# Kernel optimization log

Hardware: AMD Instinct MI355X
Metric: run time of the kernel (lower is better)

The kernel has to match this reference:

```python
import jax, jax.numpy as jnp
import numpy as np

NB, B, L, D, H = 4, 4, 1024, 512, 8
E = D // H  # head dim = 64
SCALE = 1.0 / np.sqrt(E)


def setup_inputs() -> dict:
    key = jax.random.key(0)
    ks = jax.random.split(key, 18)
    w = lambda k, shape: (jax.random.normal(k, shape, dtype=jnp.float32) * 0.02)
    inp = {
        'x': jax.random.normal(ks[0], (NB, B, L, D), dtype=jnp.float32),
        # per-block intra-attention projections, stored [in, out] (x @ W + b)
        'Wq': w(ks[1], (NB, D, D)), 'bq': w(ks[2], (NB, D)),
        'Wk': w(ks[3], (NB, D, D)), 'bk': w(ks[4], (NB, D)),
        'Wv': w(ks[5], (NB, D, D)), 'bv': w(ks[6], (NB, D)),
        'Wo': w(ks[7], (NB, D, D)), 'bo': w(ks[8], (NB, D)),
        # shared inter (router) attention projections
        'iWq': w(ks[9], (D, D)), 'ibq': w(ks[10], (D,)),
        'iWk': w(ks[11], (D, D)), 'ibk': w(ks[12], (D,)),
        'iWv': w(ks[13], (D, D)), 'ibv': w(ks[14], (D,)),
        'iWo': w(ks[15], (D, D)), 'ibo': w(ks[16], (D,)),
    }
    return inp


def _full_attn(q, k, v):
    # q,k,v: [..., S, H, E] with batch dims leading; unmasked FullAttention
    scores = jnp.einsum('...lhe,...she->...hls', q, k) * SCALE
    A = jax.nn.softmax(scores, axis=-1)
    return jnp.einsum('...hls,...shd->...lhd', A, v)


def reference(x, Wq, bq, Wk, bk, Wv, bv, Wo, bo,
              iWq, ibq, iWk, ibk, iWv, ibv, iWo, ibo):
    # ---- intra attention, vectorized over the NB blocks ----
    proj = lambda W, b: (jnp.einsum('nbld,nde->nble', x, W) + b[:, None, None, :])
    q = proj(Wq, bq).reshape(NB, B, L, H, E)
    k = proj(Wk, bk).reshape(NB, B, L, H, E)
    v = proj(Wv, bv).reshape(NB, B, L, H, E)
    o = _full_attn(q, k, v).reshape(NB, B, L, D)
    x_intra = jnp.einsum('nbld,nde->nble', o, Wo) + bo[:, None, None, :]

    # ---- inter attention over router tokens (last token of each block) ----
    routers = jnp.transpose(x_intra[:, :, -1, :], (1, 0, 2))  # [B, NB, D]
    rq = (routers @ iWq + ibq).reshape(B, NB, H, E)
    rk = (routers @ iWk + ibk).reshape(B, NB, H, E)
    rv = (routers @ iWv + ibv).reshape(B, NB, H, E)
    ro = _full_attn(rq, rk, rv).reshape(B, NB, D)
    x_inter = ro @ iWo + ibo  # [B, NB, D]

    # replace each block's last (router) token with its inter-attended version
    x_out = x_intra.at[:, :, -1, :].set(jnp.transpose(x_inter, (1, 0, 2)))
    return x_out  # [NB, B, L, D]
```

## Files before the change

### kernel.cpp

```cpp
#include <hip/hip_runtime.h>
#include <math.h>

#define NBV 4
#define BBV 4
#define LLV 1024
#define DDV 512
#define HHV 8
#define EEV 64

typedef unsigned short u16;
typedef _Float16 half8 __attribute__((ext_vector_type(8)));
typedef float f32x4 __attribute__((ext_vector_type(4)));

#define QSCALE 0.1803368801111243f

__device__ __forceinline__ u16 f2h(float f) {
  union { _Float16 h; u16 u; } v; v.h = (_Float16)f; return v.u;
}
__device__ __forceinline__ unsigned pkrtz(float a, float b) {
  typedef __fp16 fp16x2 __attribute__((ext_vector_type(2)));
  union { fp16x2 h; unsigned u; } c;
  c.h = __builtin_amdgcn_cvt_pkrtz(a, b);
  return c.u;
}
__device__ __forceinline__ void gload16(const void* g, void* l) {
  __builtin_amdgcn_global_load_lds(
      (const __attribute__((address_space(1))) unsigned int*)g,
      (__attribute__((address_space(3))) unsigned int*)l, 16, 0, 0);
}

__global__ __launch_bounds__(256) void convert(
    const float* __restrict__ x,
    const float* __restrict__ Wq, const float* __restrict__ Wk,
    const float* __restrict__ Wv, const float* __restrict__ Wo,
    u16* __restrict__ x_t, u16* __restrict__ wt, u16* __restrict__ wo)
{
  const int bid = blockIdx.x;
  if (bid < 4096) {
    const int t = bid * 256 + threadIdx.x;
    const int lane = t & 63;
    const int f = (t >> 6) & 7;
    const int kt = (t >> 9) & 15;
    const int rt = t >> 13;
    const int r = rt * 128 + f * 16 + (lane & 15);
    const int k0 = kt * 32 + (lane >> 4) * 8;
    const float* s = x + (size_t)r * 512 + k0;
    float4 v0 = *(const float4*)s;
    float4 v1 = *(const float4*)(s + 4);
    float vv[8] = {v0.x, v0.y, v0.z, v0.w, v1.x, v1.y, v1.z, v1.w};
    union { u16 s16[8]; uint4 v; } H;
#pragma unroll
    for (int j = 0; j < 8; ++j) H.s16[j] = f2h(vv[j]);
    *(uint4*)(x_t + (size_t)t * 8) = H.v;
  } else {
    const int qkv = (bid < 5632);
    const int t = (qkv ? (bid - 4096) : (bid - 5632)) * 256 + threadIdx.x;
    const int z = t >> 15;
    const int tl = t & 32767;
    const int lane = tl & 63;
    const int f = (tl >> 6) & 7;
    const int kt = (tl >> 9) & 15;
    const int rt = tl >> 13;
    const float* W;
    u16* dst;
    if (qkv) {
      const int nb = z / 3, p = z - nb * 3;
      W = (p == 0 ? Wq : p == 1 ? Wk : Wv) + (size_t)nb * 262144;
      dst = wt;
    } else {
      W = Wo + (size_t)z * 262144;
      dst = wo;
    }
    const int r = rt * 128 + f * 16 + (lane & 15);
    const int k0 = kt * 32 + (lane >> 4) * 8;
    union { u16 s16[8]; uint4 v; } H;
#pragma unroll
    for (int j = 0; j < 8; ++j) H.s16[j] = f2h(W[(size_t)(k0 + j) * 512 + r]);
    *(uint4*)(dst + (size_t)z * 262144 + (size_t)tl * 8) = H.v;
  }
}

template <int MODE>
__global__ __launch_bounds__(256) void gemm_f16(
    const u16* __restrict__ Aw, const u16* __restrict__ Bx,
    const float* __restrict__ bias0, const float* __restrict__ bias1,
    const float* __restrict__ bias2,
    u16* __restrict__ q_b, u16* __restrict__ k_b, u16* __restrict__ v_t,
    float* __restrict__ Cout)
{
  __shared__ __align__(16) u16 SM[17408];
  u16* As = SM;
  u16* Bs = SM + 4096;

  const int tid = threadIdx.x;
  const int lane = tid & 63, w = tid >> 6;
  const int l15 = lane & 15, l4 = lane >> 4;
  const int bid = blockIdx.x;

  int mt, nt, z;
  if (MODE == 0) {
    const int wgid = (bid & 7) * 192 + (bid >> 3);
    mt = wgid & 3; nt = (wgid >> 2) & 31; z = wgid >> 7;
  } else {
    const int wgid = (bid & 7) * 64 + (bid >> 3);
    mt = wgid & 31; nt = (wgid >> 5) & 3; z = wgid >> 7;
  }

  int nb, p;
  const u16 *A, *B;
  if (MODE == 0) {
    nb = z / 3; p = z - nb * 3;
    A = Aw + (size_t)z * 262144;
    B = Bx + (size_t)nb * 2097152;
  } else {
    nb = z; p = 0;
    A = Aw + (size_t)z * 2097152;
    B = Bx + (size_t)z * 262144;
  }

  const f32x4 z4 = {0.f, 0.f, 0.f, 0.f};
  f32x4 acc[4][4];
#pragma unroll
  for (int i = 0; i < 4; ++i)
#pragma unroll
    for (int j = 0; j < 4; ++j) acc[i][j] = z4;

  for (int kt = 0; kt < 16; ++kt) {
    const u16* ap = A + ((size_t)(mt * 16 + kt) * 8 + w * 2) * 512 + lane * 8;
    const u16* bp = B + ((size_t)(nt * 16 + kt) * 8 + w * 2) * 512 + lane * 8;
    __syncthreads();
    gload16(ap,       As + (w * 2 + 0) * 512);
    gload16(ap + 512, As + (w * 2 + 1) * 512);
    gload16(bp,       Bs + (w * 2 + 0) * 512);
    gload16(bp + 512, Bs + (w * 2 + 1) * 512);
    __syncthreads();

    half8 a[4], b[4];
#pragma unroll
    for (int m = 0; m < 4; ++m)
      a[m] = *(const half8*)(As + ((w >> 1) * 4 + m) * 512 + lane * 8);
#pragma unroll
    for (int n = 0; n < 4; ++n)
      b[n] = *(const half8*)(Bs + ((w & 1) * 4 + n) * 512 + lane * 8);
#pragma unroll
    for (int m = 0; m < 4; ++m)
#pragma unroll
      for (int n = 0; n < 4; ++n)
        acc[m][n] = __builtin_amdgcn_mfma_f32_16x16x32_f16(a[m], b[n], acc[m][n], 0, 0, 0);
  }

  if (MODE == 0) {
    const float* bias = (p == 0 ? bias0 : p == 1 ? bias1 : bias2) + nb * 512;
    const int hh = w >> 1;
    __syncthreads();
    if (p < 2) {
      const float scl = (p == 0) ? QSCALE : 1.0f;
#pragma unroll
      for (int mm = 0; mm < 4; ++mm) {
        const int c = mm * 4 + l4;
#pragma unroll
        for (int nn = 0; nn < 4; ++nn) {
          const int tok = (w & 1) * 64 + nn * 16 + l15;
          ushort4 pk;
#pragma unroll
          for (int i = 0; i < 4; ++i) {
            const int mf = mt * 128 + hh * 64 + mm * 16 + l4 * 4 + i;
            ((u16*)&pk)[i] = f2h((acc[mm][nn][i] + bias[mf]) * scl);
          }
          *(ushort4*)((char*)SM + hh * 17408 + tok * 136 +
                      ((c ^ (tok & 15)) * 8)) = pk;
        }
      }
      __syncthreads();
      u16* dst = (p == 0 ? q_b : k_b);
#pragma unroll
      for (int i = 0; i < 16; ++i) {
        const int idx = i * 256 + tid;
        const int h2 = idx >> 11, tok = (idx >> 4) & 127, c = idx & 15;
        ushort4 v = *(const ushort4*)((char*)SM + h2 * 17408 + tok * 136 +
                                      ((c ^ (tok & 15)) * 8));
        const int ltok = nt * 128 + tok;
        const int headf = (nb * 4 + (ltok >> 10)) * 8 + mt * 2 + h2;
        *(ushort4*)(dst + (size_t)headf * 65536 + (ltok & 1023) * 64 + c * 4) = v;
      }
    } else {
#pragma unroll
      for (int mm = 0; mm < 4; ++mm) {
#pragma unroll
        for (int nn = 0; nn < 4; ++nn) {
          const int tok = (w & 1) * 64 + nn * 16 + l15;
#pragma unroll
          for (int r = 0; r < 4; ++r) {
            const int e = mm * 16 + l4 * 4 + r;
            const int mf = mt * 128 + hh * 64 + e;
            *(u16*)((char*)SM + hh * 17408 + e * 264 + tok * 2) =
                f2h(acc[mm][nn][r] + bias[mf]);
          }
        }
      }
      __syncthreads();
#pragma unroll
      for (int i = 0; i < 16; ++i) {
        const int idx = i * 256 + tid;
        const int h2 = idx >> 11, rem = idx & 2047;
        const int e = rem >> 5, s = rem & 31;
        uint2 v = *(const uint2*)((char*)SM + h2 * 17408 + e * 264 + s * 8);
        const int headf = (nb * 4 + (nt >> 3)) * 8 + mt * 2 + h2;
        *(uint2*)(v_t + (size_t)headf * 65536 + e * 1024 +
                  (nt & 7) * 128 + s * 4) = v;
      }
    }
  } else {
#pragma unroll
    for (int mm = 0; mm < 4; ++mm) {
#pragma unroll
      for (int nn = 0; nn < 4; ++nn) {
        const int m0 = mt * 128 + ((w >> 1) * 4 + mm) * 16 + l4 * 4;
        const int n  = nt * 128 + ((w & 1) * 4 + nn) * 16 + l15;
        const float bz = bias0[nb * 512 + n];
#pragma unroll
        for (int r = 0; r < 4; ++r)
          Cout[((size_t)nb * 4096 + m0 + r) * 512 + n] = acc[mm][nn][r] + bz;
      }
    }
  }
}

__global__ __launch_bounds__(512, 4) void attn_mfma(
    const u16* __restrict__ Qb, const u16* __restrict__ Kb,
    const u16* __restrict__ Vt, u16* __restrict__ o_t)
{
  __shared__ __align__(16) u16 SM[26624];
  u16* KL = SM;
  u16* VL = SM + 8192;
  u16* PL = SM + 16384;

  const int tid = threadIdx.x;
  const int lane = tid & 63, w = tid >> 6;
  const int l15 = lane & 15, l4 = lane >> 4;
  const int sb = blockIdx.x;
  const int head = sb & 127;
  const int qt = sb >> 7;
  const size_t hbase = (size_t)head * 65536;
  const int q0 = qt * 256;

  half8 qf[2][2];
#pragma unroll
  for (int qm = 0; qm < 2; ++qm) {
    const u16* qp = Qb + hbase + (size_t)(q0 + w * 32 + qm * 16 + l15) * 64 + l4 * 8;
    qf[qm][0] = *(const half8*)qp;
    qf[qm][1] = *(const half8*)(qp + 32);
  }

  const f32x4 z4 = {0.f, 0.f, 0.f, 0.f};
  const _Float16 one_h = (_Float16)1.0f;
  const half8 ones = {one_h, one_h, one_h, one_h, one_h, one_h, one_h, one_h};
  f32x4 oacc[2][4], ls[2];
#pragma unroll
  for (int qm = 0; qm < 2; ++qm) {
    ls[qm] = z4;
#pragma unroll
    for (int ef = 0; ef < 4; ++ef) oacc[qm][ef] = z4;
  }

  const int rowl = lane >> 3;
  const int colx = ((lane & 7) ^ rowl) * 8;

#define STAGE(buf, kt0)                                                        \
  {                                                                            \
    gload16(Kb + hbase + (size_t)((kt0) + w * 8 + rowl) * 64 + colx,           \
            KL + (buf) * 4096 + w * 512);                                      \
    gload16(Vt + hbase + (size_t)(w * 8 + rowl) * 1024 + (kt0) + colx,         \
            VL + (buf) * 4096 + w * 512);                                      \
  }

  STAGE(0, 0);
  __syncthreads();

  char* Pw = (char*)(PL + w * 1280);

  for (int t = 0; t < 16; ++t) {
    const int cur = t & 1;
    if (t < 15) STAGE(cur ^ 1, (t + 1) * 64);

    f32x4 st[2][4];
#pragma unroll
    for (int qm = 0; qm < 2; ++qm)
#pragma unroll
      for (int kf = 0; kf < 4; ++kf) st[qm][kf] = z4;

    __builtin_amdgcn_s_setprio(1);
#pragma unroll
    for (int kf = 0; kf < 4; ++kf) {
      const int key = kf * 16 + l15;
      const int swz = (key & 7) << 4;
#pragma unroll
      for (int eh = 0; eh < 2; ++eh) {
        half8 af = *(const half8*)((char*)(KL + cur * 4096) +
                     ((key * 128 + eh * 64 + l4 * 16) ^ swz));
        st[0][kf] = __builtin_amdgcn_mfma_f32_16x16x32_f16(af, qf[0][eh], st[0][kf], 0, 0, 0);
        st[1][kf] = __builtin_amdgcn_mfma_f32_16x16x32_f16(af, qf[1][eh], st[1][kf], 0, 0, 0);
      }
    }
    __builtin_amdgcn_s_setprio(0);

#pragma unroll
    for (int kh = 0; kh < 2; ++kh) {
#pragma unroll
      for (int qm = 0; qm < 2; ++qm) {
        const int row = qm * 16 + l15;
#pragma unroll
        for (int kf2 = 0; kf2 < 2; ++kf2) {
          const int kf = kh * 2 + kf2;
          float e0 = __builtin_amdgcn_exp2f(st[qm][kf][0]);
          float e1 = __builtin_amdgcn_exp2f(st[qm][kf][1]);
          float e2 = __builtin_amdgcn_exp2f(st[qm][kf][2]);
          float e3 = __builtin_amdgcn_exp2f(st[qm][kf][3]);
          uint2 d;
          d.x = pkrtz(e0, e1);
          d.y = pkrtz(e2, e3);
          *(uint2*)(Pw + row * 80 + kf2 * 32 + l4 * 8) = d;
        }
      }
      __builtin_amdgcn_s_setprio(1);
      half8 pa0 = *(const half8*)(Pw + l15 * 80 + l4 * 16);
      half8 pa1 = *(const half8*)(Pw + (16 + l15) * 80 + l4 * 16);
      ls[0] = __builtin_amdgcn_mfma_f32_16x16x32_f16(pa0, ones, ls[0], 0, 0, 0);
      ls[1] = __builtin_amdgcn_mfma_f32_16x16x32_f16(pa1, ones, ls[1], 0, 0, 0);
#pragma unroll
      for (int ef = 0; ef < 4; ++ef) {
        const int e = ef * 16 + l15;
        half8 vb2 = *(const half8*)((char*)(VL + cur * 4096) +
                      ((e * 128 + kh * 64 + l4 * 16) ^ ((e & 7) << 4)));
        oacc[0][ef] = __builtin_amdgcn_mfma_f32_16x16x32_f16(pa0, vb2, oacc[0][ef], 0, 0, 0);
        oacc[1][ef] = __builtin_amdgcn_mfma_f32_16x16x32_f16(pa1, vb2, oacc[1][ef], 0, 0, 0);
      }
      __builtin_amdgcn_s_setprio(0);
    }
    __syncthreads();
  }
#undef STAGE

  char* Ot = (char*)SM;
#pragma unroll
  for (int qm = 0; qm < 2; ++qm) {
    f32x4 iv;
#pragma unroll
    for (int r = 0; r < 4; ++r) iv[r] = 1.0f / ls[qm][r];
#pragma unroll
    for (int ef = 0; ef < 4; ++ef)
#pragma unroll
      for (int r = 0; r < 4; ++r) {
        const int tokl = w * 32 + qm * 16 + l4 * 4 + r;
        const int dl = ef * 16 + l15;
        *(u16*)(Ot + ((tokl * 128 + dl * 2) ^ ((tokl & 7) << 4))) =
            f2h(oacc[qm][ef][r] * iv[r]);
      }
  }
  __syncthreads();

  const int nb = head >> 5, bb = (head >> 3) & 3, h = head & 7;
  u16* abase = o_t + (size_t)nb * 2097152;
#pragma unroll
  for (int i = 0; i < 4; ++i) {
    const int gidx = i * 512 + tid;
    const int rt_loc = gidx >> 10;
    const int rem = gidx & 1023;
    const int kh = rem >> 9, f = (rem >> 6) & 7, ln = rem & 63;
    const int tokl = rt_loc * 128 + f * 16 + (ln & 15);
    const int dl = kh * 32 + (ln >> 4) * 8;
    uint4 vvv = *(const uint4*)(Ot + ((tokl * 128 + dl * 2) ^ ((tokl & 7) << 4)));
    const int rt = bb * 8 + qt * 2 + rt_loc;
    *(uint4*)(abase + ((size_t)((rt * 16 + h * 2 + kh) * 8 + f) * 512 + ln * 8)) = vvv;
  }
}

__global__ __launch_bounds__(256) void inter_qa(
    const float* __restrict__ xout,
    const float* __restrict__ iWq, const float* __restrict__ iWk, const float* __restrict__ iWv,
    const float* __restrict__ ibq, const float* __restrict__ ibk, const float* __restrict__ ibv,
    float* __restrict__ ro)
{
    __shared__ float Rs[4][512];
    __shared__ float Pp[4][12][64];
    __shared__ float R2[3][4][64];
    const int tid = threadIdx.x;
    const int b = blockIdx.x >> 3, h = blockIdx.x & 7;

    for (int t = tid; t < 512; t += 256) {
        const int n = t >> 7, k4 = (t & 127) * 4;
        *(float4*)&Rs[n][k4] =
            *(const float4*)&xout[(((size_t)(n * BBV + b) * LLV) + (LLV - 1)) * DDV + k4];
    }
    __syncthreads();

    const int g = tid >> 6;
    const int e = tid & 63;
    const int col = h * 64 + e;
    float acc[3][4];
#pragma unroll
    for (int p = 0; p < 3; ++p)
#pragma unroll
        for (int n = 0; n < 4; ++n) acc[p][n] = 0.f;

#pragma unroll 2
    for (int kk = 0; kk < 128; ++kk) {
        const int k = g * 128 + kk;
        const float wq = iWq[(size_t)k * 512 + col];
        const float wk = iWk[(size_t)k * 512 + col];
        const float wv = iWv[(size_t)k * 512 + col];
#pragma unroll
        for (int n = 0; n < 4; ++n) {
            const float rv_ = Rs[n][k];
            acc[0][n] += rv_ * wq;
            acc[1][n] += rv_ * wk;
            acc[2][n] += rv_ * wv;
        }
    }
#pragma unroll
    for (int p = 0; p < 3; ++p)
#pragma unroll
        for (int n = 0; n < 4; ++n)
            Pp[g][p * 4 + n][e] = acc[p][n];
    __syncthreads();

#pragma unroll
    for (int p = 0; p < 3; ++p) {
        const int n = g;
        float s = Pp[0][p * 4 + n][e] + Pp[1][p * 4 + n][e] +
                  Pp[2][p * 4 + n][e] + Pp[3][p * 4 + n][e];
        const float* bias = (p == 0 ? ibq : p == 1 ? ibk : ibv);
        R2[p][n][e] = s + bias[col];
    }
    __syncthreads();

    if (tid < 64) {
        float qv[4], kv[4], vv[4];
#pragma unroll
        for (int n = 0; n < 4; ++n) {
            qv[n] = R2[0][n][tid]; kv[n] = R2[1][n][tid]; vv[n] = R2[2][n][tid];
        }
        float s[4][4];
#pragma unroll
        for (int n = 0; n < 4; ++n)
#pragma unroll
            for (int m = 0; m < 4; ++m) {
                float prod = qv[n] * kv[m];
#pragma unroll
                for (int off = 1; off < 64; off <<= 1) prod += __shfl_xor(prod, off);
                s[n][m] = prod * 0.125f;
            }
#pragma unroll
        for (int n = 0; n < 4; ++n) {
            float mx = fmaxf(fmaxf(s[n][0], s[n][1]), fmaxf(s[n][2], s[n][3]));
            float pr[4], den = 0.f, ov = 0.f;
#pragma unroll
            for (int m = 0; m < 4; ++m) { pr[m] = __expf(s[n][m] - mx); den += pr[m]; }
#pragma unroll
            for (int m = 0; m < 4; ++m) ov += pr[m] * vv[m];
            ro[(size_t)(b * 4 + n) * 512 + h * 64 + tid] = ov / den;
        }
    }
}

__global__ __launch_bounds__(256) void inter_out(
    const float* __restrict__ ro, const float* __restrict__ iWo,
    const float* __restrict__ ibo, float* __restrict__ out)
{
    __shared__ float Rs[16][512];
    __shared__ float P[16][68];
    const int tid = threadIdx.x;
    for (int t = tid; t < 2048; t += 256)
        *(float4*)&Rs[t >> 7][(t & 127) * 4] = *(const float4*)&ro[t * 4];
    __syncthreads();

    const int cb = blockIdx.x * 64;
    const int c4 = (tid & 15) * 4;
    const int kq = tid >> 4;

    f32x4 acc[16];
#pragma unroll
    for (int r = 0; r < 16; ++r) acc[r] = (f32x4){0.f, 0.f, 0.f, 0.f};

    for (int i = 0; i < 32; ++i) {
        const int k = i * 16 + kq;
        const float4 wv = *(const float4*)&iWo[(size_t)k * 512 + cb + c4];
#pragma unroll
        for (int r = 0; r < 16; ++r) {
            const float rv_ = Rs[r][k];
            acc[r][0] += rv_ * wv.x;
            acc[r][1] += rv_ * wv.y;
            acc[r][2] += rv_ * wv.z;
            acc[r][3] += rv_ * wv.w;
        }
    }

#pragma unroll
    for (int r = 0; r < 16; ++r) {
        *(f32x4*)&P[kq][c4] = acc[r];
        __syncthreads();
        if (tid < 64) {
            float s = 0.f;
#pragma unroll
            for (int q = 0; q < 16; ++q) s += P[q][tid];
            const int b = r >> 2, n = r & 3;
            out[(((size_t)(n * BBV + b) * LLV) + (LLV - 1)) * DDV + cb + tid] =
                s + ibo[cb + tid];
        }
        __syncthreads();
    }
}

extern "C" void kernel_launch(void* const* d_in, const int* in_sizes, int n_in,
                              void* d_out, int out_size, void* d_ws, size_t ws_size,
                              hipStream_t stream)
{
    (void)in_sizes; (void)n_in; (void)out_size; (void)ws_size;
    const float* x   = (const float*)d_in[0];
    const float* Wq  = (const float*)d_in[1];  const float* bq  = (const float*)d_in[2];
    const float* Wk  = (const float*)d_in[3];  const float* bk  = (const float*)d_in[4];
    const float* Wv  = (const float*)d_in[5];  const float* bv  = (const float*)d_in[6];
    const float* Wo  = (const float*)d_in[7];  const float* bo  = (const float*)d_in[8];
    const float* iWq = (const float*)d_in[9];  const float* ibq = (const float*)d_in[10];
    const float* iWk = (const float*)d_in[11]; const float* ibk = (const float*)d_in[12];
    const float* iWv = (const float*)d_in[13]; const float* ibv = (const float*)d_in[14];
    const float* iWo = (const float*)d_in[15]; const float* ibo = (const float*)d_in[16];
    float* out = (float*)d_out;

    char* W = (char*)d_ws;
    u16* x_t  = (u16*)(W);
    u16* wt   = (u16*)(W + 16777216);
    u16* wo   = (u16*)(W + 33554432);
    u16* q_b  = (u16*)(W + 35651584);
    u16* k_b  = (u16*)(W + 52428800);
    u16* v_t  = (u16*)(W + 69206016);
    u16* o_t  = (u16*)(W + 85983232);
    float* ro = (float*)(W + 102760448);

    convert<<<6144, 256, 0, stream>>>(x, Wq, Wk, Wv, Wo, x_t, wt, wo);
    gemm_f16<0><<<1536, 256, 0, stream>>>(
        wt, x_t, bq, bk, bv, q_b, k_b, v_t, nullptr);
    attn_mfma<<<512, 512, 0, stream>>>(q_b, k_b, v_t, o_t);
    gemm_f16<1><<<512, 256, 0, stream>>>(
        o_t, wo, bo, nullptr, nullptr, nullptr, nullptr, nullptr, out);
    inter_qa<<<32, 256, 0, stream>>>(out, iWq, iWk, iWv, ibq, ibk, ibv, ro);
    inter_out<<<8, 256, 0, stream>>>(ro, iWo, ibo, out);
}
```

Before: 153.4 us.

## Double GEMM k-step per barrier and restage softmax P tile with swizzle

The GEMM loop now loads two 32-wide k slices per barrier pair, which halves the number of __syncthreads and lets more MFMAs run per stage, at the cost of twice the LDS tile footprint. In attention, the whole 32x64 P tile is computed and written once into a 128-byte-row XOR-swizzled LDS buffer before the PV MFMAs. This replaces the 80-byte padded half tiles and is meant to reduce bank conflicts and interleaving stalls. LDS per attention block grows to 64KB, which may limit occupancy under the 512-thread, 4-wave launch bound.

```diff
diff --git a/kernel.cpp b/kernel.cpp
--- a/kernel.cpp
+++ b/kernel.cpp
@@ -90,7 +90,7 @@
 {
   __shared__ __align__(16) u16 SM[17408];
   u16* As = SM;
-  u16* Bs = SM + 4096;
+  u16* Bs = SM + 8192;
 
   const int tid = threadIdx.x;
   const int lane = tid & 63, w = tid >> 6;
@@ -125,28 +125,34 @@
 #pragma unroll
     for (int j = 0; j < 4; ++j) acc[i][j] = z4;
 
-  for (int kt = 0; kt < 16; ++kt) {
-    const u16* ap = A + ((size_t)(mt * 16 + kt) * 8 + w * 2) * 512 + lane * 8;
-    const u16* bp = B + ((size_t)(nt * 16 + kt) * 8 + w * 2) * 512 + lane * 8;
-    __syncthreads();
-    gload16(ap,       As + (w * 2 + 0) * 512);
-    gload16(ap + 512, As + (w * 2 + 1) * 512);
-    gload16(bp,       Bs + (w * 2 + 0) * 512);
-    gload16(bp + 512, Bs + (w * 2 + 1) * 512);
-    __syncthreads();
-
-    half8 a[4], b[4];
-#pragma unroll
-    for (int m = 0; m < 4; ++m)
-      a[m] = *(const half8*)(As + ((w >> 1) * 4 + m) * 512 + lane * 8);
-#pragma unroll
-    for (int n = 0; n < 4; ++n)
-      b[n] = *(const half8*)(Bs + ((w & 1) * 4 + n) * 512 + lane * 8);
-#pragma unroll
-    for (int m = 0; m < 4; ++m)
+  for (int kt = 0; kt < 8; ++kt) {
+    __syncthreads();
+#pragma unroll
+    for (int s = 0; s < 2; ++s) {
+      const u16* ap = A + ((size_t)((mt * 16 + kt * 2 + s) * 8) + w * 2) * 512 + lane * 8;
+      const u16* bp = B + ((size_t)((nt * 16 + kt * 2 + s) * 8) + w * 2) * 512 + lane * 8;
+      gload16(ap,       As + (s * 8 + w * 2 + 0) * 512);
+      gload16(ap + 512, As + (s * 8 + w * 2 + 1) * 512);
+      gload16(bp,       Bs + (s * 8 + w * 2 + 0) * 512);
+      gload16(bp + 512, Bs + (s * 8 + w * 2 + 1) * 512);
+    }
+    __syncthreads();
+
+#pragma unroll
+    for (int s = 0; s < 2; ++s) {
+      half8 a[4], b[4];
+#pragma unroll
+      for (int m = 0; m < 4; ++m)
+        a[m] = *(const half8*)(As + (s * 8 + (w >> 1) * 4 + m) * 512 + lane * 8);
 #pragma unroll
       for (int n = 0; n < 4; ++n)
-        acc[m][n] = __builtin_amdgcn_mfma_f32_16x16x32_f16(a[m], b[n], acc[m][n], 0, 0, 0);
+        b[n] = *(const half8*)(Bs + (s * 8 + (w & 1) * 4 + n) * 512 + lane * 8);
+#pragma unroll
+      for (int m = 0; m < 4; ++m)
+#pragma unroll
+        for (int n = 0; n < 4; ++n)
+          acc[m][n] = __builtin_amdgcn_mfma_f32_16x16x32_f16(a[m], b[n], acc[m][n], 0, 0, 0);
+    }
   }
 
   if (MODE == 0) {
@@ -230,7 +236,7 @@
     const u16* __restrict__ Qb, const u16* __restrict__ Kb,
     const u16* __restrict__ Vt, u16* __restrict__ o_t)
 {
-  __shared__ __align__(16) u16 SM[26624];
+  __shared__ __align__(16) u16 SM[32768];
   u16* KL = SM;
   u16* VL = SM + 8192;
   u16* PL = SM + 16384;
@@ -277,7 +283,7 @@
   STAGE(0, 0);
   __syncthreads();
 
-  char* Pw = (char*)(PL + w * 1280);
+  char* Pw = (char*)(PL + w * 2048);
 
   for (int t = 0; t < 16; ++t) {
     const int cur = t & 1;
@@ -305,38 +311,44 @@
     __builtin_amdgcn_s_setprio(0);
 
 #pragma unroll
+    for (int qm = 0; qm < 2; ++qm) {
+      const int rq = qm * 16 + l15;
+      const int rswz = (rq & 7) << 4;
+#pragma unroll
+      for (int kf = 0; kf < 4; ++kf) {
+        float e0 = __builtin_amdgcn_exp2f(st[qm][kf][0]);
+        float e1 = __builtin_amdgcn_exp2f(st[qm][kf][1]);
+        float e2 = __builtin_amdgcn_exp2f(st[qm][kf][2]);
+        float e3 = __builtin_amdgcn_exp2f(st[qm][kf][3]);
+        uint2 d;
+        d.x = pkrtz(e0, e1);
+        d.y = pkrtz(e2, e3);
+        *(uint2*)(Pw + ((rq * 128 + kf * 32 + l4 * 8) ^ rswz)) = d;
+      }
+    }
+
+    __builtin_amdgcn_s_setprio(1);
+#pragma unroll
     for (int kh = 0; kh < 2; ++kh) {
+      half8 pa[2];
 #pragma unroll
       for (int qm = 0; qm < 2; ++qm) {
-        const int row = qm * 16 + l15;
-#pragma unroll
-        for (int kf2 = 0; kf2 < 2; ++kf2) {
-          const int kf = kh * 2 + kf2;
-          float e0 = __builtin_amdgcn_exp2f(st[qm][kf][0]);
-          float e1 = __builtin_amdgcn_exp2f(st[qm][kf][1]);
-          float e2 = __builtin_amdgcn_exp2f(st[qm][kf][2]);
-          float e3 = __builtin_amdgcn_exp2f(st[qm][kf][3]);
-          uint2 d;
-          d.x = pkrtz(e0, e1);
-          d.y = pkrtz(e2, e3);
-          *(uint2*)(Pw + row * 80 + kf2 * 32 + l4 * 8) = d;
-        }
-      }
-      __builtin_amdgcn_s_setprio(1);
-      half8 pa0 = *(const half8*)(Pw + l15 * 80 + l4 * 16);
-      half8 pa1 = *(const half8*)(Pw + (16 + l15) * 80 + l4 * 16);
-      ls[0] = __builtin_amdgcn_mfma_f32_16x16x32_f16(pa0, ones, ls[0], 0, 0, 0);
-      ls[1] = __builtin_amdgcn_mfma_f32_16x16x32_f16(pa1, ones, ls[1], 0, 0, 0);
+        const int rq = qm * 16 + l15;
+        pa[qm] = *(const half8*)(Pw +
+                   ((rq * 128 + kh * 64 + l4 * 16) ^ ((rq & 7) << 4)));
+      }
+      ls[0] = __builtin_amdgcn_mfma_f32_16x16x32_f16(pa[0], ones, ls[0], 0, 0, 0);
+      ls[1] = __builtin_amdgcn_mfma_f32_16x16x32_f16(pa[1], ones, ls[1], 0, 0, 0);
 #pragma unroll
       for (int ef = 0; ef < 4; ++ef) {
         const int e = ef * 16 + l15;
         half8 vb2 = *(const half8*)((char*)(VL + cur * 4096) +
                       ((e * 128 + kh * 64 + l4 * 16) ^ ((e & 7) << 4)));
-        oacc[0][ef] = __builtin_amdgcn_mfma_f32_16x16x32_f16(pa0, vb2, oacc[0][ef], 0, 0, 0);
-        oacc[1][ef] = __builtin_amdgcn_mfma_f32_16x16x32_f16(pa1, vb2, oacc[1][ef], 0, 0, 0);
-      }
-      __builtin_amdgcn_s_setprio(0);
-    }
+        oacc[0][ef] = __builtin_amdgcn_mfma_f32_16x16x32_f16(pa[0], vb2, oacc[0][ef], 0, 0, 0);
+        oacc[1][ef] = __builtin_amdgcn_mfma_f32_16x16x32_f16(pa[1], vb2, oacc[1][ef], 0, 0, 0);
+      }
+    }
+    __builtin_amdgcn_s_setprio(0);
     __syncthreads();
   }
 #undef STAGE
```

After: 154.3 us. About the same (+0.6%).
